# Performance work log

Measured on AMD Instinct MI355X. Metric: run time of the kernel, lower is better.

The kernel has to match this reference:

```python
import jax, jax.numpy as jnp
import numpy as np

B, T, E, H, C = 256, 512, 256, 256, 6
FORGET_BIAS = 1.0


def _lstm_step(c, h, x, W, b):
    # TF LSTMCell: z = [x, h] @ W + b, gates ordered (i, j, f, o)
    z = jnp.concatenate([x, h], axis=-1) @ W + b
    i, j, f, o = jnp.split(z, 4, axis=-1)
    c_new = c * jax.nn.sigmoid(f + FORGET_BIAS) + jax.nn.sigmoid(i) * jnp.tanh(j)
    h_new = jnp.tanh(c_new) * jax.nn.sigmoid(o)
    return c_new, h_new


def setup_inputs() -> dict:
    key = jax.random.key(0)
    ks = jax.random.split(key, 4)
    x = jax.random.normal(ks[0], (B, T, E), dtype=jnp.float32)
    # tf.random_normal_initializer for head weights; LSTM kernels ~ glorot-ish scale
    W1 = jax.random.normal(ks[1], (E + H, 4 * H), dtype=jnp.float32) * 0.05
    b1 = jnp.zeros((4 * H,), dtype=jnp.float32)
    W2 = jax.random.normal(ks[2], (H + H, 4 * H), dtype=jnp.float32) * 0.05
    b2 = jnp.zeros((4 * H,), dtype=jnp.float32)
    W_out = jax.random.normal(ks[3], (H, C), dtype=jnp.float32)
    b_out = jnp.zeros((C,), dtype=jnp.float32)
    return {"x": x, "W1": W1, "b1": b1, "W2": W2, "b2": b2,
            "W_out": W_out, "b_out": b_out}


def reference(x, W1, b1, W2, b2, W_out, b_out):
    # 2-layer LSTM over time via lax.scan (zero initial state), then
    # dense + sigmoid + 0.5 threshold head applied to every timestep output.
    def step(carry, x_t):
        c1, h1, c2, h2 = carry
        c1, h1 = _lstm_step(c1, h1, x_t, W1, b1)
        c2, h2 = _lstm_step(c2, h2, h1, W2, b2)
        return (c1, h1, c2, h2), h2

    zeros = jnp.zeros((x.shape[0], H), dtype=x.dtype)
    init = (zeros, zeros, zeros, zeros)
    xs = jnp.swapaxes(x, 0, 1)  # [T, B, E]
    _, outs = jax.lax.scan(step, init, xs)  # outs: [T, B, H]
    outs = jnp.swapaxes(outs, 0, 1).reshape(-1, H)  # [B*T, H]

    logits = outs @ W_out + b_out  # [B*T, C]
    probs = jax.nn.sigmoid(logits)
    condition = 0.5 < probs
    prediction = jnp.where(condition, jnp.ones_like(probs), jnp.zeros_like(probs))
    return logits, condition, prediction
```

## Files before the change

### kernel.cpp

```cpp
#include <hip/hip_runtime.h>
#include <math.h>

#define T_ 512

__device__ __forceinline__ float sigf(float x) {
  return __builtin_amdgcn_rcpf(1.0f + __expf(-x));
}
__device__ __forceinline__ float tanhf_(float x) {
  float e = __expf(x + x);
  return 1.0f - 2.0f * __builtin_amdgcn_rcpf(e + 1.0f);
}

__device__ __forceinline__ float hloadf(const float* p) {
  unsigned u = __hip_atomic_load((const unsigned*)p,
                                 __ATOMIC_RELAXED, __HIP_MEMORY_SCOPE_AGENT);
  return __builtin_bit_cast(float, u);
}
__device__ __forceinline__ void hstoref(float* p, float v) {
  __hip_atomic_store((unsigned*)p, __builtin_bit_cast(unsigned, v),
                     __ATOMIC_RELAXED, __HIP_MEMORY_SCOPE_AGENT);
}

__device__ __forceinline__ int aoff_f(int kc) { return (kc << 3) + ((kc >> 6) << 2); }

__global__ __launch_bounds__(512, 1) void lstm2_head(
    const float* __restrict__ x, const float* __restrict__ W1,
    const float* __restrict__ b1, const float* __restrict__ W2,
    const float* __restrict__ b2, const float* __restrict__ Wo,
    const float* __restrict__ bo, float* __restrict__ out,
    unsigned char* __restrict__ ws)
{
  __shared__ float Alds[6192];
  __shared__ float zbuf[2112];

  const int tid = threadIdx.x;
  const int g  = blockIdx.x >> 3;
  const int w  = blockIdx.x & 7;
  const int rb0 = g << 3;

  unsigned* bar = (unsigned*)ws + (g << 4);
  float* hbase = (float*)(ws + 4096);
  float* h1g = hbase + (size_t)g * 4096;
  float* h2g = hbase + 131072 + (size_t)g * 4096;

  for (int i = tid; i < 4096; i += 512) { hstoref(h1g + i, 0.0f); hstoref(h2g + i, 0.0f); }

  __builtin_amdgcn_s_waitcnt(0);
  __syncthreads();
  if (tid == 0) {
    __hip_atomic_fetch_add(bar, 1u, __ATOMIC_RELAXED, __HIP_MEMORY_SCOPE_AGENT);
    while (__hip_atomic_load(bar, __ATOMIC_RELAXED, __HIP_MEMORY_SCOPE_AGENT) < 8u) {}
    __asm__ volatile("" ::: "memory");
  }
  __syncthreads();

  const int lane = tid & 63;
  const int wvid = tid >> 6;
  const int half = wvid >> 2;
  const int gate = wvid & 3;
  const int kt   = lane >> 3;
  const int og   = lane & 7;
  const bool b5 = (lane & 32) != 0;
  const bool b4 = (lane & 16) != 0;
  const bool b3 = (lane & 8) != 0;
  const float* wbase = (half ? W2 : W1)
      + (size_t)(kt << 6) * 1024 + (gate << 8) + (w << 5) + (og << 2);
  const int kc0  = (half << 8) + (kt << 6);
  const int zrow = ((half << 2) + gate) << 3;

  const int sr  = tid & 7;
  const int skc = tid >> 3;

  const int L  = tid >> 8;
  const int ur = (tid >> 5) & 7;
  const int hj = tid & 31;
  const float* ubb = L ? b2 : b1;
  const int ucol = (w << 5) + hj;
  const float ub_i = ubb[ucol];
  const float ub_j = ubb[256 + ucol];
  const float ub_f = ubb[512 + ucol] + 1.0f;
  const float ub_o = ubb[768 + ucol];
  double cst = 0.0;

  const bool headblk = (w == 0);
  float wo_r[4][6];
  float bo_r[6];
  if (headblk) {
    #pragma unroll
    for (int q = 0; q < 4; ++q)
      #pragma unroll
      for (int c = 0; c < 6; ++c) wo_r[q][c] = Wo[(lane + (q << 6)) * 6 + c];
    #pragma unroll
    for (int c = 0; c < 6; ++c) bo_r[c] = bo[c];
  }

  auto do_head = [&](int t3) {
    float pr[6] = {0, 0, 0, 0, 0, 0};
    #pragma unroll
    for (int q = 0; q < 4; ++q) {
      float hv = Alds[aoff_f(512 + lane + (q << 6)) + wvid];
      #pragma unroll
      for (int c = 0; c < 6; ++c) pr[c] = fmaf(hv, wo_r[q][c], pr[c]);
    }
    #pragma unroll
    for (int off = 1; off <= 32; off <<= 1)
      #pragma unroll
      for (int c = 0; c < 6; ++c) pr[c] += __shfl_xor(pr[c], off, 64);
    if (lane == 0) {
      size_t orow = (((size_t)(rb0 + wvid)) << 9) + (size_t)t3;
      #pragma unroll
      for (int c = 0; c < 6; ++c) {
        float lg = pr[c] + bo_r[c];
        out[orow * 6 + c] = lg;
        float pd = (lg > 0.0f) ? 1.0f : 0.0f;
        out[(size_t)786432 + orow * 6 + c] = pd;
        out[(size_t)1572864 + orow * 6 + c] = pd;
      }
    }
  };

  {
    const float* xb = x + (size_t)(rb0 + sr) * (T_ * 256) + skc;
    float sv[12];
    #pragma unroll
    for (int v = 0; v < 4; ++v) sv[v] = xb[v << 6];
    const float* h1p = h1g + 2048;
    const float* h2p = h2g;
    #pragma unroll
    for (int v = 0; v < 4; ++v) sv[4 + v] = hloadf(h1p + (sr << 8) + skc + (v << 6));
    #pragma unroll
    for (int v = 0; v < 4; ++v) sv[8 + v] = hloadf(h2p + (sr << 8) + skc + (v << 6));
    #pragma unroll
    for (int v = 0; v < 12; ++v) Alds[aoff_f((v << 6) + skc) + sr] = sv[v];
  }
  __syncthreads();

  float4 wva[8];
  #pragma unroll
  for (int j = 0; j < 8; ++j) wva[j] = *(const float4*)(wbase + (size_t)j * 1024);

  #pragma unroll 1
  for (int p = 0; p <= T_ + 1; ++p) {
    float acc[4][8];
    #pragma unroll
    for (int c = 0; c < 4; ++c)
      #pragma unroll
      for (int r = 0; r < 8; ++r) acc[c][r] = 0.0f;
    {
      const float* ap = Alds + aoff_f(kc0);
      float4 wvb[8];
      #pragma unroll 1
      for (int sg = 0; sg < 4; ++sg) {
        const int s0 = sg << 4;
        #pragma unroll
        for (int j = 0; j < 8; ++j)
          wvb[j] = *(const float4*)(wbase + (size_t)(s0 + 8 + j) * 1024);
        #pragma unroll
        for (int j = 0; j < 8; ++j) {
          const float* apj = ap + ((s0 + j) << 3);
          float4 a0 = *(const float4*)(apj);
          float4 a1 = *(const float4*)(apj + 4);
          float a[8] = {a0.x, a0.y, a0.z, a0.w, a1.x, a1.y, a1.z, a1.w};
          #pragma unroll
          for (int r = 0; r < 8; ++r) {
            acc[0][r] = fmaf(a[r], wva[j].x, acc[0][r]);
            acc[1][r] = fmaf(a[r], wva[j].y, acc[1][r]);
            acc[2][r] = fmaf(a[r], wva[j].z, acc[2][r]);
            acc[3][r] = fmaf(a[r], wva[j].w, acc[3][r]);
          }
        }
        if (sg < 3) {
          #pragma unroll
          for (int j = 0; j < 8; ++j)
            wva[j] = *(const float4*)(wbase + (size_t)(s0 + 16 + j) * 1024);
        }
        #pragma unroll
        for (int j = 0; j < 8; ++j) {
          const float* apj = ap + ((s0 + 8 + j) << 3);
          float4 a0 = *(const float4*)(apj);
          float4 a1 = *(const float4*)(apj + 4);
          float a[8] = {a0.x, a0.y, a0.z, a0.w, a1.x, a1.y, a1.z, a1.w};
          #pragma unroll
          for (int r = 0; r < 8; ++r) {
            acc[0][r] = fmaf(a[r], wvb[j].x, acc[0][r]);
            acc[1][r] = fmaf(a[r], wvb[j].y, acc[1][r]);
            acc[2][r] = fmaf(a[r], wvb[j].z, acc[2][r]);
            acc[3][r] = fmaf(a[r], wvb[j].w, acc[3][r]);
          }
        }
      }
    }

    float tA[4][4];
    #pragma unroll
    for (int c = 0; c < 4; ++c)
      #pragma unroll
      for (int q = 0; q < 4; ++q) {
        float send = b5 ? acc[c][q] : acc[c][q + 4];
        float keep = b5 ? acc[c][q + 4] : acc[c][q];
        tA[c][q] = keep + __shfl_xor(send, 32, 64);
      }
    float tB[4][2];
    #pragma unroll
    for (int c = 0; c < 4; ++c)
      #pragma unroll
      for (int q = 0; q < 2; ++q) {
        float send = b4 ? tA[c][q] : tA[c][q + 2];
        float keep = b4 ? tA[c][q + 2] : tA[c][q];
        tB[c][q] = keep + __shfl_xor(send, 16, 64);
      }
    #pragma unroll
    for (int c = 0; c < 4; ++c) {
      float send = b3 ? tB[c][0] : tB[c][1];
      float keep = b3 ? tB[c][1] : tB[c][0];
      float zv = keep + __shfl_xor(send, 8, 64);
      zbuf[(zrow + kt) * 33 + (og << 2) + c] = zv;
    }
    __syncthreads();

    {
      const bool uact = L ? (p >= 1 && p <= T_) : (p < T_);
      if (uact) {
        const float* za = zbuf + ((L << 5) + ur) * 33 + hj;
        float si = sigf(za[0]   + ub_i);
        float tj = tanhf_(za[264] + ub_j);
        float sf = sigf(za[528] + ub_f);
        float so = sigf(za[792] + ub_o);
        cst = cst * (double)sf + (double)(si * tj);
        float hv = tanhf_((float)cst) * so;
        float* hd = L ? (h2g + (((p + 1) & 1) << 11)) : (h1g + ((p & 1) << 11));
        hstoref(hd + (ur << 8) + ucol, hv);
      }
    }

    if (p <= T_) {
      if (headblk && p >= 2) do_head(p - 2);

      __builtin_amdgcn_s_waitcnt(0);
      __syncthreads();
      if (tid == 0)
        __hip_atomic_fetch_add(bar, 1u, __ATOMIC_RELAXED, __HIP_MEMORY_SCOPE_AGENT);

      const int xp1 = (p + 1 < T_) ? (p + 1) : (T_ - 1);
      const float* xb = x + (size_t)(rb0 + sr) * (T_ * 256) + (size_t)xp1 * 256 + skc;
      float xv[4];
      #pragma unroll
      for (int v = 0; v < 4; ++v) xv[v] = xb[v << 6];
      #pragma unroll
      for (int v = 0; v < 4; ++v) Alds[aoff_f((v << 6) + skc) + sr] = xv[v];

      #pragma unroll
      for (int j = 0; j < 8; ++j) wva[j] = *(const float4*)(wbase + (size_t)j * 1024);

      if (tid == 0) {
        const unsigned target = ((unsigned)(p + 2)) << 3;
        while (__hip_atomic_load(bar, __ATOMIC_RELAXED, __HIP_MEMORY_SCOPE_AGENT) < target) {}
        __asm__ volatile("" ::: "memory");
      }
      __syncthreads();

      const float* h1p = h1g + ((p & 1) << 11);
      const float* h2p = h2g + (((p + 1) & 1) << 11);
      float hv8[8];
      #pragma unroll
      for (int v = 0; v < 4; ++v) hv8[v] = hloadf(h1p + (sr << 8) + skc + (v << 6));
      #pragma unroll
      for (int v = 0; v < 4; ++v) hv8[4 + v] = hloadf(h2p + (sr << 8) + skc + (v << 6));
      #pragma unroll
      for (int v = 0; v < 8; ++v) Alds[aoff_f(256 + (v << 6) + skc) + sr] = hv8[v];
      __syncthreads();
    } else {
      if (headblk) do_head(p - 2);
    }
  }
}

extern "C" void kernel_launch(void* const* d_in, const int* in_sizes, int n_in,
                              void* d_out, int out_size, void* d_ws, size_t ws_size,
                              hipStream_t stream) {
  const float* x  = (const float*)d_in[0];
  const float* W1 = (const float*)d_in[1];
  const float* b1 = (const float*)d_in[2];
  const float* W2 = (const float*)d_in[3];
  const float* b2 = (const float*)d_in[4];
  const float* Wo = (const float*)d_in[5];
  const float* bo = (const float*)d_in[6];
  float* out = (float*)d_out;
  unsigned char* ws = (unsigned char*)d_ws;

  hipMemsetAsync(d_ws, 0, 4096, stream);

  lstm2_head<<<dim3(256), dim3(512), 0, stream>>>(x, W1, b1, W2, b2, Wo, bo, out, ws);
}
```

Measured before the change: 6.125 ms.

## Regroup LSTM into 16-row groups with register-resident weight slices

Changes the cooperative grid from 32 groups of 8 blocks to 16 groups of 16 blocks. Each block now owns 16 batch rows and 16 hidden columns, and keeps its full weight slice (32 float4 per thread) in registers instead of re-streaming weights from global memory every timestep. Shuffle reductions, the LDS layout and the head are adapted to match. The aim is to remove the per-step weight reload traffic. The cost is much higher register pressure and 16-way cross-block barriers, and the launch site (not shown) must supply the matching grid size.

After: 22.29 ms. +264.0%, slower.

```diff
diff --git a/kernel.cpp b/kernel.cpp
--- a/kernel.cpp
+++ b/kernel.cpp
@@ -21,7 +21,7 @@
                      __ATOMIC_RELAXED, __HIP_MEMORY_SCOPE_AGENT);
 }
 
-__device__ __forceinline__ int aoff_f(int kc) { return (kc << 3) + ((kc >> 6) << 2); }
+__device__ __forceinline__ int aoff16(int kc) { return (kc << 4) + ((kc >> 5) << 2); }
 
 __global__ __launch_bounds__(512, 1) void lstm2_head(
     const float* __restrict__ x, const float* __restrict__ W1,
@@ -30,26 +30,26 @@
     const float* __restrict__ bo, float* __restrict__ out,
     unsigned char* __restrict__ ws)
 {
-  __shared__ float Alds[6192];
-  __shared__ float zbuf[2112];
+  __shared__ float Alds[12384];
+  __shared__ float zbuf[2176];
 
   const int tid = threadIdx.x;
-  const int g  = blockIdx.x >> 3;
-  const int w  = blockIdx.x & 7;
-  const int rb0 = g << 3;
+  const int g  = blockIdx.x >> 4;
+  const int w  = blockIdx.x & 15;
+  const int rb0 = g << 4;
 
   unsigned* bar = (unsigned*)ws + (g << 4);
   float* hbase = (float*)(ws + 4096);
-  float* h1g = hbase + (size_t)g * 4096;
-  float* h2g = hbase + 131072 + (size_t)g * 4096;
-
-  for (int i = tid; i < 4096; i += 512) { hstoref(h1g + i, 0.0f); hstoref(h2g + i, 0.0f); }
+  float* h1g = hbase + (size_t)g * 8192;
+  float* h2g = hbase + 131072 + (size_t)g * 8192;
+
+  for (int i = tid; i < 8192; i += 512) { hstoref(h1g + i, 0.0f); hstoref(h2g + i, 0.0f); }
 
   __builtin_amdgcn_s_waitcnt(0);
   __syncthreads();
   if (tid == 0) {
     __hip_atomic_fetch_add(bar, 1u, __ATOMIC_RELAXED, __HIP_MEMORY_SCOPE_AGENT);
-    while (__hip_atomic_load(bar, __ATOMIC_RELAXED, __HIP_MEMORY_SCOPE_AGENT) < 8u) {}
+    while (__hip_atomic_load(bar, __ATOMIC_RELAXED, __HIP_MEMORY_SCOPE_AGENT) < 16u) {}
     __asm__ volatile("" ::: "memory");
   }
   __syncthreads();
@@ -58,24 +58,32 @@
   const int wvid = tid >> 6;
   const int half = wvid >> 2;
   const int gate = wvid & 3;
-  const int kt   = lane >> 3;
-  const int og   = lane & 7;
-  const bool b5 = (lane & 32) != 0;
-  const bool b4 = (lane & 16) != 0;
-  const bool b3 = (lane & 8) != 0;
-  const float* wbase = (half ? W2 : W1)
-      + (size_t)(kt << 6) * 1024 + (gate << 8) + (w << 5) + (og << 2);
-  const int kc0  = (half << 8) + (kt << 6);
-  const int zrow = ((half << 2) + gate) << 3;
-
-  const int sr  = tid & 7;
-  const int skc = tid >> 3;
+  const int kt   = lane >> 2;
+  const int og   = lane & 3;
+  const bool q5 = (lane & 32) != 0;
+  const bool q4 = (lane & 16) != 0;
+  const bool q3 = (lane & 8)  != 0;
+  const bool q2 = (lane & 4)  != 0;
+  const float* Wp = half ? W2 : W1;
+  const int colb = (gate << 8) + (w << 4) + (og << 2);
+
+  float4 wc[32];
+  #pragma unroll
+  for (int s = 0; s < 32; ++s)
+    wc[s] = *(const float4*)(Wp + (size_t)((kt << 5) + s) * 1024 + colb);
+
+  const int abase = aoff16((half << 8) + (kt << 5));
+  const int zrow  = (((half << 2) + gate) << 4) + kt;
+
+  const int sr  = tid & 15;
+  const int skg = tid >> 4;
+  const int sc0 = skg << 3;
 
   const int L  = tid >> 8;
-  const int ur = (tid >> 5) & 7;
-  const int hj = tid & 31;
+  const int ur = (tid >> 4) & 15;
+  const int uc = tid & 15;
   const float* ubb = L ? b2 : b1;
-  const int ucol = (w << 5) + hj;
+  const int ucol = (w << 4) + uc;
   const float ub_i = ubb[ucol];
   const float ub_j = ubb[256 + ucol];
   const float ub_f = ubb[512 + ucol] + 1.0f;
@@ -83,191 +91,179 @@
   double cst = 0.0;
 
   const bool headblk = (w == 0);
-  float wo_r[4][6];
-  float bo_r[6];
-  if (headblk) {
+
+  auto do_head = [&](int t3) {
+    float wo_r[4][6];
+    float bo_r[6];
     #pragma unroll
     for (int q = 0; q < 4; ++q)
       #pragma unroll
       for (int c = 0; c < 6; ++c) wo_r[q][c] = Wo[(lane + (q << 6)) * 6 + c];
     #pragma unroll
     for (int c = 0; c < 6; ++c) bo_r[c] = bo[c];
-  }
-
-  auto do_head = [&](int t3) {
-    float pr[6] = {0, 0, 0, 0, 0, 0};
-    #pragma unroll
-    for (int q = 0; q < 4; ++q) {
-      float hv = Alds[aoff_f(512 + lane + (q << 6)) + wvid];
-      #pragma unroll
-      for (int c = 0; c < 6; ++c) pr[c] = fmaf(hv, wo_r[q][c], pr[c]);
-    }
-    #pragma unroll
-    for (int off = 1; off <= 32; off <<= 1)
-      #pragma unroll
-      for (int c = 0; c < 6; ++c) pr[c] += __shfl_xor(pr[c], off, 64);
-    if (lane == 0) {
-      size_t orow = (((size_t)(rb0 + wvid)) << 9) + (size_t)t3;
-      #pragma unroll
-      for (int c = 0; c < 6; ++c) {
-        float lg = pr[c] + bo_r[c];
-        out[orow * 6 + c] = lg;
-        float pd = (lg > 0.0f) ? 1.0f : 0.0f;
-        out[(size_t)786432 + orow * 6 + c] = pd;
-        out[(size_t)1572864 + orow * 6 + c] = pd;
+    #pragma unroll
+    for (int rr = 0; rr < 2; ++rr) {
+      const int r = (wvid << 1) + rr;
+      float pr[6] = {0, 0, 0, 0, 0, 0};
+      #pragma unroll
+      for (int q = 0; q < 4; ++q) {
+        float hv = Alds[aoff16(512 + lane + (q << 6)) + r];
+        #pragma unroll
+        for (int c = 0; c < 6; ++c) pr[c] = fmaf(hv, wo_r[q][c], pr[c]);
+      }
+      #pragma unroll
+      for (int off = 1; off <= 32; off <<= 1)
+        #pragma unroll
+        for (int c = 0; c < 6; ++c) pr[c] += __shfl_xor(pr[c], off, 64);
+      if (lane == 0) {
+        size_t orow = (((size_t)(rb0 + r)) << 9) + (size_t)t3;
+        #pragma unroll
+        for (int c = 0; c < 6; ++c) {
+          float lg = pr[c] + bo_r[c];
+          out[orow * 6 + c] = lg;
+          float pd = (lg > 0.0f) ? 1.0f : 0.0f;
+          out[(size_t)786432 + orow * 6 + c] = pd;
+          out[(size_t)1572864 + orow * 6 + c] = pd;
+        }
       }
     }
   };
 
   {
-    const float* xb = x + (size_t)(rb0 + sr) * (T_ * 256) + skc;
-    float sv[12];
-    #pragma unroll
-    for (int v = 0; v < 4; ++v) sv[v] = xb[v << 6];
-    const float* h1p = h1g + 2048;
+    const float* xb = x + (size_t)(rb0 + sr) * (T_ * 256) + sc0;
+    float sv[8];
+    #pragma unroll
+    for (int j = 0; j < 8; ++j) sv[j] = xb[j];
+    #pragma unroll
+    for (int j = 0; j < 8; ++j) Alds[aoff16(sc0 + j) + sr] = sv[j];
+    const float* h1p = h1g + 4096;
     const float* h2p = h2g;
-    #pragma unroll
-    for (int v = 0; v < 4; ++v) sv[4 + v] = hloadf(h1p + (sr << 8) + skc + (v << 6));
-    #pragma unroll
-    for (int v = 0; v < 4; ++v) sv[8 + v] = hloadf(h2p + (sr << 8) + skc + (v << 6));
-    #pragma unroll
-    for (int v = 0; v < 12; ++v) Alds[aoff_f((v << 6) + skc) + sr] = sv[v];
+    float hv[16];
+    #pragma unroll
+    for (int j = 0; j < 8; ++j) hv[j]     = hloadf(h1p + (sr << 8) + sc0 + j);
+    #pragma unroll
+    for (int j = 0; j < 8; ++j) hv[8 + j] = hloadf(h2p + (sr << 8) + sc0 + j);
+    #pragma unroll
+    for (int j = 0; j < 8; ++j) Alds[aoff16(256 + sc0 + j) + sr] = hv[j];
+    #pragma unroll
+    for (int j = 0; j < 8; ++j) Alds[aoff16(512 + sc0 + j) + sr] = hv[8 + j];
   }
   __syncthreads();
 
-  float4 wva[8];
-  #pragma unroll
-  for (int j = 0; j < 8; ++j) wva[j] = *(const float4*)(wbase + (size_t)j * 1024);
-
   #pragma unroll 1
   for (int p = 0; p <= T_ + 1; ++p) {
-    float acc[4][8];
-    #pragma unroll
-    for (int c = 0; c < 4; ++c)
-      #pragma unroll
-      for (int r = 0; r < 8; ++r) acc[c][r] = 0.0f;
+    float acc[4][16];
+    #pragma unroll
+    for (int c = 0; c < 4; ++c)
+      #pragma unroll
+      for (int r = 0; r < 16; ++r) acc[c][r] = 0.0f;
     {
-      const float* ap = Alds + aoff_f(kc0);
-      float4 wvb[8];
-      #pragma unroll 1
-      for (int sg = 0; sg < 4; ++sg) {
-        const int s0 = sg << 4;
-        #pragma unroll
-        for (int j = 0; j < 8; ++j)
-          wvb[j] = *(const float4*)(wbase + (size_t)(s0 + 8 + j) * 1024);
-        #pragma unroll
-        for (int j = 0; j < 8; ++j) {
-          const float* apj = ap + ((s0 + j) << 3);
-          float4 a0 = *(const float4*)(apj);
-          float4 a1 = *(const float4*)(apj + 4);
-          float a[8] = {a0.x, a0.y, a0.z, a0.w, a1.x, a1.y, a1.z, a1.w};
-          #pragma unroll
-          for (int r = 0; r < 8; ++r) {
-            acc[0][r] = fmaf(a[r], wva[j].x, acc[0][r]);
-            acc[1][r] = fmaf(a[r], wva[j].y, acc[1][r]);
-            acc[2][r] = fmaf(a[r], wva[j].z, acc[2][r]);
-            acc[3][r] = fmaf(a[r], wva[j].w, acc[3][r]);
-          }
+      const float* ap = Alds + abase;
+      #pragma unroll
+      for (int s = 0; s < 32; ++s) {
+        const float* as = ap + (s << 4);
+        float4 a0 = *(const float4*)(as);
+        float4 a1 = *(const float4*)(as + 4);
+        float4 a2 = *(const float4*)(as + 8);
+        float4 a3 = *(const float4*)(as + 12);
+        float a[16] = {a0.x, a0.y, a0.z, a0.w, a1.x, a1.y, a1.z, a1.w,
+                       a2.x, a2.y, a2.z, a2.w, a3.x, a3.y, a3.z, a3.w};
+        #pragma unroll
+        for (int r = 0; r < 16; ++r) {
+          acc[0][r] = fmaf(a[r], wc[s].x, acc[0][r]);
+          acc[1][r] = fmaf(a[r], wc[s].y, acc[1][r]);
+          acc[2][r] = fmaf(a[r], wc[s].z, acc[2][r]);
+          acc[3][r] = fmaf(a[r], wc[s].w, acc[3][r]);
         }
-        if (sg < 3) {
-          #pragma unroll
-          for (int j = 0; j < 8; ++j)
-            wva[j] = *(const float4*)(wbase + (size_t)(s0 + 16 + j) * 1024);
-        }
-        #pragma unroll
-        for (int j = 0; j < 8; ++j) {
-          const float* apj = ap + ((s0 + 8 + j) << 3);
-          float4 a0 = *(const float4*)(apj);
-          float4 a1 = *(const float4*)(apj + 4);
-          float a[8] = {a0.x, a0.y, a0.z, a0.w, a1.x, a1.y, a1.z, a1.w};
-          #pragma unroll
-          for (int r = 0; r < 8; ++r) {
-            acc[0][r] = fmaf(a[r], wvb[j].x, acc[0][r]);
-            acc[1][r] = fmaf(a[r], wvb[j].y, acc[1][r]);
-            acc[2][r] = fmaf(a[r], wvb[j].z, acc[2][r]);
-            acc[3][r] = fmaf(a[r], wvb[j].w, acc[3][r]);
-          }
-        }
-      }
-    }
-
-    float tA[4][4];
+      }
+    }
+
+    float t1[4][8];
+    #pragma unroll
+    for (int c = 0; c < 4; ++c)
+      #pragma unroll
+      for (int q = 0; q < 8; ++q) {
+        float send = q5 ? acc[c][q] : acc[c][q + 8];
+        float keep = q5 ? acc[c][q + 8] : acc[c][q];
+        t1[c][q] = keep + __shfl_xor(send, 32, 64);
+      }
+    float t2[4][4];
     #pragma unroll
     for (int c = 0; c < 4; ++c)
       #pragma unroll
       for (int q = 0; q < 4; ++q) {
-        float send = b5 ? acc[c][q] : acc[c][q + 4];
-        float keep = b5 ? acc[c][q + 4] : acc[c][q];
-        tA[c][q] = keep + __shfl_xor(send, 32, 64);
-      }
-    float tB[4][2];
+        float send = q4 ? t1[c][q] : t1[c][q + 4];
+        float keep = q4 ? t1[c][q + 4] : t1[c][q];
+        t2[c][q] = keep + __shfl_xor(send, 16, 64);
+      }
+    float t3[4][2];
     #pragma unroll
     for (int c = 0; c < 4; ++c)
       #pragma unroll
       for (int q = 0; q < 2; ++q) {
-        float send = b4 ? tA[c][q] : tA[c][q + 2];
-        float keep = b4 ? tA[c][q + 2] : tA[c][q];
-        tB[c][q] = keep + __shfl_xor(send, 16, 64);
+        float send = q3 ? t2[c][q] : t2[c][q + 2];
+        float keep = q3 ? t2[c][q + 2] : t2[c][q];
+        t3[c][q] = keep + __shfl_xor(send, 8, 64);
       }
     #pragma unroll
     for (int c = 0; c < 4; ++c) {
-      float send = b3 ? tB[c][0] : tB[c][1];
-      float keep = b3 ? tB[c][1] : tB[c][0];
-      float zv = keep + __shfl_xor(send, 8, 64);
-      zbuf[(zrow + kt) * 33 + (og << 2) + c] = zv;
+      float send = q2 ? t3[c][0] : t3[c][1];
+      float keep = q2 ? t3[c][1] : t3[c][0];
+      float zv = keep + __shfl_xor(send, 4, 64);
+      zbuf[zrow * 17 + (og << 2) + c] = zv;
     }
     __syncthreads();
 
     {
       const bool uact = L ? (p >= 1 && p <= T_) : (p < T_);
       if (uact) {
-        const float* za = zbuf + ((L << 5) + ur) * 33 + hj;
+        const float* za = zbuf + ((L << 6) + ur) * 17 + uc;
         float si = sigf(za[0]   + ub_i);
-        float tj = tanhf_(za[264] + ub_j);
-        float sf = sigf(za[528] + ub_f);
-        float so = sigf(za[792] + ub_o);
+        float tj = tanhf_(za[272] + ub_j);
+        float sf = sigf(za[544] + ub_f);
+        float so = sigf(za[816] + ub_o);
         cst = cst * (double)sf + (double)(si * tj);
         float hv = tanhf_((float)cst) * so;
-        float* hd = L ? (h2g + (((p + 1) & 1) << 11)) : (h1g + ((p & 1) << 11));
+        float* hd = L ? (h2g + (((p + 1) & 1) << 12)) : (h1g + ((p & 1) << 12));
         hstoref(hd + (ur << 8) + ucol, hv);
       }
     }
 
     if (p <= T_) {
-      if (headblk && p >= 2) do_head(p - 2);
-
       __builtin_amdgcn_s_waitcnt(0);
       __syncthreads();
       if (tid == 0)
         __hip_atomic_fetch_add(bar, 1u, __ATOMIC_RELAXED, __HIP_MEMORY_SCOPE_AGENT);
 
       const int xp1 = (p + 1 < T_) ? (p + 1) : (T_ - 1);
-      const float* xb = x + (size_t)(rb0 + sr) * (T_ * 256) + (size_t)xp1 * 256 + skc;
-      float xv[4];
-      #pragma unroll
-      for (int v = 0; v < 4; ++v) xv[v] = xb[v << 6];
-      #pragma unroll
-      for (int v = 0; v < 4; ++v) Alds[aoff_f((v << 6) + skc) + sr] = xv[v];
-
-      #pragma unroll
-      for (int j = 0; j < 8; ++j) wva[j] = *(const float4*)(wbase + (size_t)j * 1024);
+      const float* xb = x + (size_t)(rb0 + sr) * (T_ * 256) + (size_t)xp1 * 256 + sc0;
+      float xv[8];
+      #pragma unroll
+      for (int j = 0; j < 8; ++j) xv[j] = xb[j];
+
+      if (headblk && p >= 2) do_head(p - 2);
+
+      #pragma unroll
+      for (int j = 0; j < 8; ++j) Alds[aoff16(sc0 + j) + sr] = xv[j];
 
       if (tid == 0) {
-        const unsigned target = ((unsigned)(p + 2)) << 3;
+        const unsigned target = ((unsigned)(p + 2)) << 4;
         while (__hip_atomic_load(bar, __ATOMIC_RELAXED, __HIP_MEMORY_SCOPE_AGENT) < target) {}
         __asm__ volatile("" ::: "memory");
       }
       __syncthreads();
 
-      const float* h1p = h1g + ((p & 1) << 11);
-      const float* h2p = h2g + (((p + 1) & 1) << 11);
-      float hv8[8];
-      #pragma unroll
-      for (int v = 0; v < 4; ++v) hv8[v] = hloadf(h1p + (sr << 8) + skc + (v << 6));
-      #pragma unroll
-      for (int v = 0; v < 4; ++v) hv8[4 + v] = hloadf(h2p + (sr << 8) + skc + (v << 6));
-      #pragma unroll
-      for (int v = 0; v < 8; ++v) Alds[aoff_f(256 + (v << 6) + skc) + sr] = hv8[v];
+      const float* h1p = h1g + ((p & 1) << 12);
+      const float* h2p = h2g + (((p + 1) & 1) << 12);
+      float hv[16];
+      #pragma unroll
+      for (int j = 0; j < 8; ++j) hv[j]     = hloadf(h1p + (sr << 8) + sc0 + j);
+      #pragma unroll
+      for (int j = 0; j < 8; ++j) hv[8 + j] = hloadf(h2p + (sr << 8) + sc0 + j);
+      #pragma unroll
+      for (int j = 0; j < 8; ++j) Alds[aoff16(256 + sc0 + j) + sr] = hv[j];
+      #pragma unroll
+      for (int j = 0; j < 8; ++j) Alds[aoff16(512 + sc0 + j) + sr] = hv[8 + j];
       __syncthreads();
     } else {
       if (headblk) do_head(p - 2);
```

## Split each batch group across 16 blocks instead of 8 to halve per-block work

Applied to the files above, without the earlier changes.

Each group of 8 batch rows now spreads its gate columns over 16 cooperating blocks (512 blocks total), so each block handles 16 hidden columns and half the K-loop iterations, with an extra cross-lane reduction stage and a smaller z buffer. Launch bounds allow two blocks per CU, and the head weights are loaded inside the head routine to free registers. The aim is to shorten the per-timestep critical path of the recurrent matmul. The cost is a grid barrier spanning twice as many blocks, more atomic traffic, and half the update threads sitting idle.

Measured after the change: 10.41 ms. +69.9%, slower.

```diff
diff --git a/kernel.cpp b/kernel.cpp
--- a/kernel.cpp
+++ b/kernel.cpp
@@ -21,21 +21,21 @@
                      __ATOMIC_RELAXED, __HIP_MEMORY_SCOPE_AGENT);
 }
 
-__device__ __forceinline__ int aoff_f(int kc) { return (kc << 3) + ((kc >> 6) << 2); }
-
-__global__ __launch_bounds__(512, 1) void lstm2_head(
+__device__ __forceinline__ int aoff8(int kc) { return (kc << 3) + ((kc >> 5) << 2); }
+
+__global__ __launch_bounds__(512, 2) void lstm2_head(
     const float* __restrict__ x, const float* __restrict__ W1,
     const float* __restrict__ b1, const float* __restrict__ W2,
     const float* __restrict__ b2, const float* __restrict__ Wo,
     const float* __restrict__ bo, float* __restrict__ out,
     unsigned char* __restrict__ ws)
 {
-  __shared__ float Alds[6192];
-  __shared__ float zbuf[2112];
+  __shared__ float Alds[6240];
+  __shared__ float zbuf[1088];
 
   const int tid = threadIdx.x;
-  const int g  = blockIdx.x >> 3;
-  const int w  = blockIdx.x & 7;
+  const int g  = blockIdx.x >> 4;
+  const int w  = blockIdx.x & 15;
   const int rb0 = g << 3;
 
   unsigned* bar = (unsigned*)ws + (g << 4);
@@ -49,7 +49,7 @@
   __syncthreads();
   if (tid == 0) {
     __hip_atomic_fetch_add(bar, 1u, __ATOMIC_RELAXED, __HIP_MEMORY_SCOPE_AGENT);
-    while (__hip_atomic_load(bar, __ATOMIC_RELAXED, __HIP_MEMORY_SCOPE_AGENT) < 8u) {}
+    while (__hip_atomic_load(bar, __ATOMIC_RELAXED, __HIP_MEMORY_SCOPE_AGENT) < 16u) {}
     __asm__ volatile("" ::: "memory");
   }
   __syncthreads();
@@ -58,24 +58,28 @@
   const int wvid = tid >> 6;
   const int half = wvid >> 2;
   const int gate = wvid & 3;
-  const int kt   = lane >> 3;
-  const int og   = lane & 7;
+  const int kt   = lane >> 2;
+  const int og   = lane & 3;
   const bool b5 = (lane & 32) != 0;
   const bool b4 = (lane & 16) != 0;
-  const bool b3 = (lane & 8) != 0;
-  const float* wbase = (half ? W2 : W1)
-      + (size_t)(kt << 6) * 1024 + (gate << 8) + (w << 5) + (og << 2);
-  const int kc0  = (half << 8) + (kt << 6);
-  const int zrow = ((half << 2) + gate) << 3;
+  const bool b3 = (lane & 8)  != 0;
+  const bool b2b = (lane & 4) != 0;
+  const float* Wp = half ? W2 : W1;
+  const float* wbase = Wp + (size_t)(kt << 5) * 1024
+                          + (gate << 8) + (w << 4) + (og << 2);
+  const int abase = aoff8((half << 8) + (kt << 5));
+  const int zrowb = ((half << 2) + gate) << 3;
 
   const int sr  = tid & 7;
   const int skc = tid >> 3;
 
   const int L  = tid >> 8;
-  const int ur = (tid >> 5) & 7;
-  const int hj = tid & 31;
+  const int rem = tid & 255;
+  const int ur = (rem >> 4) & 7;
+  const int uc = rem & 15;
+  const bool ucell = rem < 128;
   const float* ubb = L ? b2 : b1;
-  const int ucol = (w << 5) + hj;
+  const int ucol = (w << 4) + uc;
   const float ub_i = ubb[ucol];
   const float ub_j = ubb[256 + ucol];
   const float ub_f = ubb[512 + ucol] + 1.0f;
@@ -83,22 +87,20 @@
   double cst = 0.0;
 
   const bool headblk = (w == 0);
-  float wo_r[4][6];
-  float bo_r[6];
-  if (headblk) {
+
+  auto do_head = [&](int t3) {
+    float wo_r[4][6];
+    float bo_r[6];
     #pragma unroll
     for (int q = 0; q < 4; ++q)
       #pragma unroll
       for (int c = 0; c < 6; ++c) wo_r[q][c] = Wo[(lane + (q << 6)) * 6 + c];
     #pragma unroll
     for (int c = 0; c < 6; ++c) bo_r[c] = bo[c];
-  }
-
-  auto do_head = [&](int t3) {
     float pr[6] = {0, 0, 0, 0, 0, 0};
     #pragma unroll
     for (int q = 0; q < 4; ++q) {
-      float hv = Alds[aoff_f(512 + lane + (q << 6)) + wvid];
+      float hv = Alds[aoff8(512 + lane + (q << 6)) + wvid];
       #pragma unroll
       for (int c = 0; c < 6; ++c) pr[c] = fmaf(hv, wo_r[q][c], pr[c]);
     }
@@ -131,7 +133,7 @@
     #pragma unroll
     for (int v = 0; v < 4; ++v) sv[8 + v] = hloadf(h2p + (sr << 8) + skc + (v << 6));
     #pragma unroll
-    for (int v = 0; v < 12; ++v) Alds[aoff_f((v << 6) + skc) + sr] = sv[v];
+    for (int v = 0; v < 12; ++v) Alds[aoff8((v << 6) + skc) + sr] = sv[v];
   }
   __syncthreads();
 
@@ -147,10 +149,10 @@
       #pragma unroll
       for (int r = 0; r < 8; ++r) acc[c][r] = 0.0f;
     {
-      const float* ap = Alds + aoff_f(kc0);
+      const float* ap = Alds + abase;
       float4 wvb[8];
       #pragma unroll 1
-      for (int sg = 0; sg < 4; ++sg) {
+      for (int sg = 0; sg < 2; ++sg) {
         const int s0 = sg << 4;
         #pragma unroll
         for (int j = 0; j < 8; ++j)
@@ -169,7 +171,7 @@
             acc[3][r] = fmaf(a[r], wva[j].w, acc[3][r]);
           }
         }
-        if (sg < 3) {
+        if (sg < 1) {
           #pragma unroll
           for (int j = 0; j < 8; ++j)
             wva[j] = *(const float4*)(wbase + (size_t)(s0 + 16 + j) * 1024);
@@ -191,41 +193,52 @@
       }
     }
 
-    float tA[4][4];
+    float t1[4][4];
     #pragma unroll
     for (int c = 0; c < 4; ++c)
       #pragma unroll
       for (int q = 0; q < 4; ++q) {
         float send = b5 ? acc[c][q] : acc[c][q + 4];
         float keep = b5 ? acc[c][q + 4] : acc[c][q];
-        tA[c][q] = keep + __shfl_xor(send, 32, 64);
-      }
-    float tB[4][2];
+        t1[c][q] = keep + __shfl_xor(send, 32, 64);
+      }
+    float t2[4][2];
     #pragma unroll
     for (int c = 0; c < 4; ++c)
       #pragma unroll
       for (int q = 0; q < 2; ++q) {
-        float send = b4 ? tA[c][q] : tA[c][q + 2];
-        float keep = b4 ? tA[c][q + 2] : tA[c][q];
-        tB[c][q] = keep + __shfl_xor(send, 16, 64);
-      }
+        float send = b4 ? t1[c][q] : t1[c][q + 2];
+        float keep = b4 ? t1[c][q + 2] : t1[c][q];
+        t2[c][q] = keep + __shfl_xor(send, 16, 64);
+      }
+    float t3v[4];
     #pragma unroll
     for (int c = 0; c < 4; ++c) {
-      float send = b3 ? tB[c][0] : tB[c][1];
-      float keep = b3 ? tB[c][1] : tB[c][0];
-      float zv = keep + __shfl_xor(send, 8, 64);
-      zbuf[(zrow + kt) * 33 + (og << 2) + c] = zv;
+      float send = b3 ? t2[c][0] : t2[c][1];
+      float keep = b3 ? t2[c][1] : t2[c][0];
+      t3v[c] = keep + __shfl_xor(send, 8, 64);
+    }
+    {
+      float send0 = b2b ? t3v[0] : t3v[2];
+      float send1 = b2b ? t3v[1] : t3v[3];
+      float keep0 = b2b ? t3v[2] : t3v[0];
+      float keep1 = b2b ? t3v[3] : t3v[1];
+      float z0 = keep0 + __shfl_xor(send0, 4, 64);
+      float z1 = keep1 + __shfl_xor(send1, 4, 64);
+      const int zi = (zrowb + (kt >> 1)) * 17 + (og << 2) + ((kt & 1) << 1);
+      zbuf[zi]     = z0;
+      zbuf[zi + 1] = z1;
     }
     __syncthreads();
 
     {
-      const bool uact = L ? (p >= 1 && p <= T_) : (p < T_);
+      const bool uact = ucell && (L ? (p >= 1 && p <= T_) : (p < T_));
       if (uact) {
-        const float* za = zbuf + ((L << 5) + ur) * 33 + hj;
+        const float* za = zbuf + ((L << 5) + ur) * 17 + uc;
         float si = sigf(za[0]   + ub_i);
-        float tj = tanhf_(za[264] + ub_j);
-        float sf = sigf(za[528] + ub_f);
-        float so = sigf(za[792] + ub_o);
+        float tj = tanhf_(za[136] + ub_j);
+        float sf = sigf(za[272] + ub_f);
+        float so = sigf(za[408] + ub_o);
         cst = cst * (double)sf + (double)(si * tj);
         float hv = tanhf_((float)cst) * so;
         float* hd = L ? (h2g + (((p + 1) & 1) << 11)) : (h1g + ((p & 1) << 11));
@@ -247,13 +260,13 @@
       #pragma unroll
       for (int v = 0; v < 4; ++v) xv[v] = xb[v << 6];
       #pragma unroll
-      for (int v = 0; v < 4; ++v) Alds[aoff_f((v << 6) + skc) + sr] = xv[v];
+      for (int v = 0; v < 4; ++v) Alds[aoff8((v << 6) + skc) + sr] = xv[v];
 
       #pragma unroll
       for (int j = 0; j < 8; ++j) wva[j] = *(const float4*)(wbase + (size_t)j * 1024);
 
       if (tid == 0) {
-        const unsigned target = ((unsigned)(p + 2)) << 3;
+        const unsigned target = ((unsigned)(p + 2)) << 4;
         while (__hip_atomic_load(bar, __ATOMIC_RELAXED, __HIP_MEMORY_SCOPE_AGENT) < target) {}
         __asm__ volatile("" ::: "memory");
       }
@@ -267,7 +280,7 @@
       #pragma unroll
       for (int v = 0; v < 4; ++v) hv8[4 + v] = hloadf(h2p + (sr << 8) + skc + (v << 6));
       #pragma unroll
-      for (int v = 0; v < 8; ++v) Alds[aoff_f(256 + (v << 6) + skc) + sr] = hv8[v];
+      for (int v = 0; v < 8; ++v) Alds[aoff8(256 + (v << 6) + skc) + sr] = hv8[v];
       __syncthreads();
     } else {
       if (headblk) do_head(p - 2);
@@ -290,5 +303,5 @@
 
   hipMemsetAsync(d_ws, 0, 4096, stream);
 
-  lstm2_head<<<dim3(256), dim3(512), 0, stream>>>(x, W1, b1, W2, b2, Wo, bo, out, ws);
-}
+  lstm2_head<<<dim3(512), dim3(512), 0, stream>>>(x, W1, b1, W2, b2, Wo, bo, out, ws);
+}
```
